# Kernel optimization log

Measured on AMD Instinct MI355X. Metric: run time of the kernel, lower is better.

## Reference

```python
import jax, jax.numpy as jnp
import numpy as np

B = 512
IN_CORES = 12      # input_eff_capsules = 3072/256
N_PRIM = 12        # num_primary_capsules
N_PAR = 10         # num_parent_capsules
RFPC = 4           # receptive fields per capsule = 256/64
RF = 64            # receptive field size
CAP = 256          # capsule size
P_CONN = 0.2


def setup_inputs() -> dict:
    key = jax.random.key(0)
    ks = jax.random.split(key, 16)
    x = jax.random.uniform(ks[0], (B, 32, 32, 3), dtype=jnp.float32)
    # sparse 0/1 routing tensors (fixed Bernoulli(p) connectivity, stored as float params)
    C1 = jax.random.bernoulli(ks[1], P_CONN, (IN_CORES, RFPC, N_PRIM, RFPC)).astype(jnp.float32)
    C_skip = jax.random.bernoulli(ks[2], P_CONN, (IN_CORES, RFPC, N_PAR, RFPC)).astype(jnp.float32)
    C2 = jax.random.bernoulli(ks[3], P_CONN, (N_PRIM, RFPC, N_PAR, RFPC)).astype(jnp.float32)
    # per-receptive-field linear weights of the capsule layers
    s = 1.0 / np.sqrt(RF)
    W1 = jax.random.normal(ks[4], (N_PRIM, RFPC, RF, RF), dtype=jnp.float32) * s
    b1 = jnp.zeros((N_PRIM, RFPC, RF), dtype=jnp.float32)
    W2 = jax.random.normal(ks[5], (N_PAR, RFPC, RF, RF), dtype=jnp.float32) * s
    b2 = jnp.zeros((N_PAR, RFPC, RF), dtype=jnp.float32)
    # reconstruction MLP: 2560 -> 5000 -> 4000 -> 3072
    Wr1 = jax.random.normal(ks[6], (2560, 5000), dtype=jnp.float32) * (1.0 / np.sqrt(2560))
    br1 = jnp.zeros((5000,), dtype=jnp.float32)
    Wr2 = jax.random.normal(ks[7], (5000, 4000), dtype=jnp.float32) * (1.0 / np.sqrt(5000))
    br2 = jnp.zeros((4000,), dtype=jnp.float32)
    Wr3 = jax.random.normal(ks[8], (4000, 3072), dtype=jnp.float32) * (1.0 / np.sqrt(4000))
    br3 = jnp.zeros((3072,), dtype=jnp.float32)
    return {"x": x, "C1": C1, "W1": W1, "b1": b1, "C_skip": C_skip,
            "C2": C2, "W2": W2, "b2": b2,
            "Wr1": Wr1, "br1": br1, "Wr2": Wr2, "br2": br2, "Wr3": Wr3, "br3": br3}


def _caps_layer(x_flat, C, W, b):
    # x_flat: (B, in_cores*RFPC*RF); C: (in_cores, RFPC, out_caps, RFPC)
    bsz = x_flat.shape[0]
    in_cores = C.shape[0]
    xr = x_flat.reshape(bsz, in_cores, RFPC, RF)
    routed = jnp.einsum('ijkl,bijm->bklm', C, xr)          # (B, out_caps, RFPC, RF)
    out = jax.nn.relu(jnp.einsum('bklm,klmn->bkln', routed, W) + b)
    return out.reshape(bsz, -1)


def reference(x, C1, W1, b1, C_skip, C2, W2, b2, Wr1, br1, Wr2, br2, Wr3, br3):
    bsz = x.shape[0]
    # spatial_block_reshape: pure reshapes -> flatten
    x_flat = x.reshape(bsz, -1)                             # (B, 3072)
    # primary capsule layer
    x_prim = _caps_layer(x_flat, C1, W1, b1)                # (B, 3072)
    # skip connection: sparse routing einsum input->parent
    xr = x_prim.reshape(bsz, IN_CORES, RFPC, RF)
    x_skip = jnp.einsum('ijkl,bijm->bklm', C_skip, xr).reshape(bsz, -1)  # (B, 2560)
    # parent capsule layer + skip
    x_sum = x_skip + _caps_layer(x_prim, C2, W2, b2)        # (B, 2560)
    # top-1 capsule mask by norm
    norms = jnp.linalg.norm(x_sum.reshape(bsz, N_PAR, CAP), axis=-1)  # (B, 10)
    active = jnp.argmax(norms, axis=-1)                     # (B,)
    cap_id = jnp.arange(N_PAR * CAP) // CAP                 # (2560,)
    mask = (cap_id[None, :] == active[:, None]).astype(x_sum.dtype)
    x_recon = mask * x_sum
    # reconstruction MLP
    h = jax.nn.relu(x_recon @ Wr1 + br1)
    h = jax.nn.relu(h @ Wr2 + br2)
    out = jax.nn.sigmoid(h @ Wr3 + br3)                     # (B, 3072)
    return (out, x_sum)
```

## Files before the change

### kernel.cpp

```cpp
#include <hip/hip_runtime.h>
#include <math.h>


#define BATCH 512
#define OUT0_SZ (512*3072)

#define LD_XREC 2576
#define LD_H1 5136
#define LD_H2 4112
#define LDP2 4224
#define LDP3 3200
#define SPLITK 4

typedef __attribute__((ext_vector_type(8))) short short8;
typedef __attribute__((ext_vector_type(4))) float f32x4;

__device__ inline unsigned short f2bf(float f) {
    union { float f; unsigned u; } v; v.f = f;
    unsigned r = v.u + 0x7fffu + ((v.u >> 16) & 1u);
    return (unsigned short)(r >> 16);
}
__device__ inline float bf2f(unsigned int hi16) {
    union { unsigned u; float f; } v; v.u = hi16 << 16; return v.f;
}

#define GLD16(g, l) __builtin_amdgcn_global_load_lds( \
    (const __attribute__((address_space(1))) unsigned int*)(g), \
    (__attribute__((address_space(3))) unsigned int*)(l), 16, 0, 0)

struct BReg { float4 r0, r1, r2, r3; };

__device__ inline void loadB(BReg& br, const float* B, int ldB, int Kr, int Nr,
                             int k0, int bn, int tid)
{
    int kq = tid >> 5, f4c = tid & 31;
    int ka = k0 + kq * 4;
    int nb = bn + f4c * 4;
    float4 z = make_float4(0.f, 0.f, 0.f, 0.f);
    br.r0 = z; br.r1 = z; br.r2 = z; br.r3 = z;
    const float* p = B + (size_t)ka * ldB + nb;
    if (nb + 3 < Nr) {
        if (ka + 3 < Kr) {
            br.r0 = *(const float4*)p;
            br.r1 = *(const float4*)(p + ldB);
            br.r2 = *(const float4*)(p + 2 * (size_t)ldB);
            br.r3 = *(const float4*)(p + 3 * (size_t)ldB);
        } else {
            if (ka     < Kr) br.r0 = *(const float4*)p;
            if (ka + 1 < Kr) br.r1 = *(const float4*)(p + ldB);
            if (ka + 2 < Kr) br.r2 = *(const float4*)(p + 2 * (size_t)ldB);
            if (ka + 3 < Kr) br.r3 = *(const float4*)(p + 3 * (size_t)ldB);
        }
    } else {
        float t[4][4] = {};
        #pragma unroll
        for (int e = 0; e < 4; ++e)
            if (ka + e < Kr)
                #pragma unroll
                for (int j = 0; j < 4; ++j)
                    if (nb + j < Nr) t[e][j] = B[(size_t)(ka + e) * ldB + nb + j];
        br.r0 = make_float4(t[0][0], t[0][1], t[0][2], t[0][3]);
        br.r1 = make_float4(t[1][0], t[1][1], t[1][2], t[1][3]);
        br.r2 = make_float4(t[2][0], t[2][1], t[2][2], t[2][3]);
        br.r3 = make_float4(t[3][0], t[3][1], t[3][2], t[3][3]);
    }
}

__device__ inline void writeB(const BReg& br, unsigned short* Bs, int tid)
{
    int kq = tid >> 5, f4c = tid & 31;
    int kqs = kq ^ ((f4c & 3) << 1);
    uint2* B2 = (uint2*)Bs;
    float a0[4] = {br.r0.x, br.r0.y, br.r0.z, br.r0.w};
    float a1[4] = {br.r1.x, br.r1.y, br.r1.z, br.r1.w};
    float a2[4] = {br.r2.x, br.r2.y, br.r2.z, br.r2.w};
    float a3[4] = {br.r3.x, br.r3.y, br.r3.z, br.r3.w};
    #pragma unroll
    for (int j = 0; j < 4; ++j) {
        unsigned int u0 = (unsigned)f2bf(a0[j]) | ((unsigned)f2bf(a1[j]) << 16);
        unsigned int u1 = (unsigned)f2bf(a2[j]) | ((unsigned)f2bf(a3[j]) << 16);
        B2[(f4c * 4 + j) * 10 + kqs] = make_uint2(u0, u1);
    }
}

__device__ inline short8 readB(const unsigned short* Bs, int n, int q)
{
    int sw = ((n >> 2) & 3) << 1;
    return *(const short8*)&Bs[n * 40 + ((2 * q) ^ sw) * 4];
}

__global__ __launch_bounds__(256) void conv_small(
    const float* __restrict__ W1, unsigned short* __restrict__ W1t,
    const float* __restrict__ W2, unsigned short* __restrict__ W2t)
{
    int bid = blockIdx.x;
    const float* W; unsigned short* Wt;
    if (bid < 48) { W = W1 + (size_t)bid * 4096; Wt = W1t + (size_t)bid * 4096; }
    else          { W = W2 + (size_t)(bid - 48) * 4096; Wt = W2t + (size_t)(bid - 48) * 4096; }
    int tid = threadIdx.x;
    int nr = tid >> 2;
    int kc = (tid & 3) * 16;
    float v[16];
    #pragma unroll
    for (int i = 0; i < 16; ++i)
        v[i] = W[(size_t)(kc + i) * 64 + nr];
    unsigned int u[8];
    #pragma unroll
    for (int j = 0; j < 8; ++j)
        u[j] = (unsigned int)f2bf(v[2 * j]) | ((unsigned int)f2bf(v[2 * j + 1]) << 16);
    unsigned int* dst = (unsigned int*)&Wt[(size_t)nr * 64 + kc];
    *(uint4*)(dst)     = make_uint4(u[0], u[1], u[2], u[3]);
    *(uint4*)(dst + 4) = make_uint4(u[4], u[5], u[6], u[7]);
}

__global__ __launch_bounds__(256) void caps_gemm1(
    const float* __restrict__ x, const float* __restrict__ C1,
    const unsigned short* __restrict__ W1t, const float* __restrict__ b1,
    unsigned short* __restrict__ xp)
{
    __shared__ __align__(16) unsigned short As[128 * 72];
    __shared__ __align__(16) unsigned short Bs[64 * 72];
    __shared__ float Csh[48];
    int kl = blockIdx.x;
    int bm = blockIdx.y * 128;
    int tid = threadIdx.x;
    int w = tid >> 6, lane = tid & 63, q = lane >> 4, r16 = lane & 15;
    int wm = (w >> 1) * 64, wn = (w & 1) * 32;

    if (tid < 48) Csh[tid] = C1[tid * 48 + kl];
    {
        const uint4* src = (const uint4*)(W1t + (size_t)kl * 4096);
        #pragma unroll
        for (int p = 0; p < 2; ++p) {
            int c = tid + p * 256;
            int row = c >> 3, cq = c & 7;
            *(uint4*)&Bs[row * 72 + cq * 8] = src[c];
        }
    }
    __syncthreads();

    int arow = tid >> 1, ah = (tid & 1) * 32;
    float accp[32];
    #pragma unroll
    for (int i = 0; i < 32; ++i) accp[i] = 0.f;
    const float* xrow = x + (size_t)(bm + arow) * 3072 + ah;
    for (int ij = 0; ij < 48; ++ij) {
        float c = Csh[ij];
        if (c != 0.f) {
            const float4* p4 = (const float4*)(xrow + ij * 64);
            #pragma unroll
            for (int cc = 0; cc < 8; ++cc) {
                float4 v = p4[cc];
                accp[cc * 4 + 0] = fmaf(c, v.x, accp[cc * 4 + 0]);
                accp[cc * 4 + 1] = fmaf(c, v.y, accp[cc * 4 + 1]);
                accp[cc * 4 + 2] = fmaf(c, v.z, accp[cc * 4 + 2]);
                accp[cc * 4 + 3] = fmaf(c, v.w, accp[cc * 4 + 3]);
            }
        }
    }
    {
        unsigned short* dst = &As[arow * 72 + ah];
        #pragma unroll
        for (int cc = 0; cc < 4; ++cc) {
            unsigned int u[4];
            #pragma unroll
            for (int j = 0; j < 4; ++j)
                u[j] = (unsigned int)f2bf(accp[cc * 8 + 2 * j]) |
                       ((unsigned int)f2bf(accp[cc * 8 + 2 * j + 1]) << 16);
            *(uint4*)&dst[cc * 8] = make_uint4(u[0], u[1], u[2], u[3]);
        }
    }
    __syncthreads();

    f32x4 acc[4][2];
    #pragma unroll
    for (int i = 0; i < 4; ++i)
        #pragma unroll
        for (int j = 0; j < 2; ++j) acc[i][j] = (f32x4)0.f;
    #pragma unroll
    for (int ks = 0; ks < 2; ++ks) {
        short8 a[4], b[2];
        #pragma unroll
        for (int mt = 0; mt < 4; ++mt)
            a[mt] = *(const short8*)&As[(wm + mt * 16 + r16) * 72 + ks * 32 + q * 8];
        #pragma unroll
        for (int nt = 0; nt < 2; ++nt)
            b[nt] = *(const short8*)&Bs[(wn + nt * 16 + r16) * 72 + ks * 32 + q * 8];
        #pragma unroll
        for (int mt = 0; mt < 4; ++mt)
            #pragma unroll
            for (int nt = 0; nt < 2; ++nt)
                acc[mt][nt] = __builtin_amdgcn_mfma_f32_16x16x32_bf16(a[mt], b[nt], acc[mt][nt], 0, 0, 0);
    }

    #pragma unroll
    for (int mt = 0; mt < 4; ++mt) {
        #pragma unroll
        for (int nt = 0; nt < 2; ++nt) {
            int n = wn + nt * 16 + r16;
            float bv = b1[kl * 64 + n];
            #pragma unroll
            for (int reg = 0; reg < 4; ++reg) {
                int row = bm + wm + mt * 16 + q * 4 + reg;
                xp[(size_t)row * 3072 + kl * 64 + n] = f2bf(fmaxf(acc[mt][nt][reg] + bv, 0.f));
            }
        }
    }
}

__global__ __launch_bounds__(256) void caps_gemm2(
    const unsigned short* __restrict__ xp, const float* __restrict__ Cs,
    const float* __restrict__ C2, const unsigned short* __restrict__ W2t,
    const float* __restrict__ b2, float* __restrict__ xsum,
    float* __restrict__ part8)
{
    __shared__ __align__(16) unsigned short As[128 * 72];
    __shared__ __align__(16) unsigned short Bs[64 * 72];
    __shared__ float C2sh[48], Cssh[48];
    int kl = blockIdx.x;
    int bm = blockIdx.y * 128;
    int tid = threadIdx.x;
    int w = tid >> 6, lane = tid & 63, q = lane >> 4, r16 = lane & 15;
    int wm = (w >> 1) * 64, wn = (w & 1) * 32;
    int half = w & 1;

    if (tid < 48) { C2sh[tid] = C2[tid * 40 + kl]; Cssh[tid] = Cs[tid * 40 + kl]; }
    {
        const uint4* src = (const uint4*)(W2t + (size_t)kl * 4096);
        #pragma unroll
        for (int p = 0; p < 2; ++p) {
            int c = tid + p * 256;
            int row = c >> 3, cq = c & 7;
            *(uint4*)&Bs[row * 72 + cq * 8] = src[c];
        }
    }
    __syncthreads();

    int arow = tid >> 1, ah = (tid & 1) * 32;
    float accp[32], skp[32];
    #pragma unroll
    for (int i = 0; i < 32; ++i) { accp[i] = 0.f; skp[i] = 0.f; }
    const unsigned short* xprow = xp + (size_t)(bm + arow) * 3072 + ah;
    for (int ij = 0; ij < 48; ++ij) {
        float c2 = C2sh[ij], cs = Cssh[ij];
        if (c2 != 0.f || cs != 0.f) {
            const uint4* p4 = (const uint4*)(xprow + ij * 64);
            #pragma unroll
            for (int cc = 0; cc < 4; ++cc) {
                uint4 v = p4[cc];
                unsigned int uu[4] = {v.x, v.y, v.z, v.w};
                #pragma unroll
                for (int j = 0; j < 4; ++j) {
                    float lo = bf2f(uu[j] & 0xffffu);
                    float hi = bf2f(uu[j] >> 16);
                    int idx = cc * 8 + 2 * j;
                    accp[idx]     = fmaf(c2, lo, accp[idx]);
                    accp[idx + 1] = fmaf(c2, hi, accp[idx + 1]);
                    skp[idx]      = fmaf(cs, lo, skp[idx]);
                    skp[idx + 1]  = fmaf(cs, hi, skp[idx + 1]);
                }
            }
        }
    }
    {
        unsigned short* dst = &As[arow * 72 + ah];
        #pragma unroll
        for (int cc = 0; cc < 4; ++cc) {
            unsigned int u[4];
            #pragma unroll
            for (int j = 0; j < 4; ++j)
                u[j] = (unsigned int)f2bf(accp[cc * 8 + 2 * j]) |
                       ((unsigned int)f2bf(accp[cc * 8 + 2 * j + 1]) << 16);
            *(uint4*)&dst[cc * 8] = make_uint4(u[0], u[1], u[2], u[3]);
        }
        float* sx = xsum + (size_t)(bm + arow) * 2560 + kl * 64 + ah;
        #pragma unroll
        for (int cc = 0; cc < 8; ++cc)
            *(float4*)&sx[cc * 4] = make_float4(skp[cc*4], skp[cc*4+1], skp[cc*4+2], skp[cc*4+3]);
    }
    __syncthreads();

    f32x4 acc[4][2];
    #pragma unroll
    for (int i = 0; i < 4; ++i)
        #pragma unroll
        for (int j = 0; j < 2; ++j) acc[i][j] = (f32x4)0.f;
    #pragma unroll
    for (int ks = 0; ks < 2; ++ks) {
        short8 a[4], b[2];
        #pragma unroll
        for (int mt = 0; mt < 4; ++mt)
            a[mt] = *(const short8*)&As[(wm + mt * 16 + r16) * 72 + ks * 32 + q * 8];
        #pragma unroll
        for (int nt = 0; nt < 2; ++nt)
            b[nt] = *(const short8*)&Bs[(wn + nt * 16 + r16) * 72 + ks * 32 + q * 8];
        #pragma unroll
        for (int mt = 0; mt < 4; ++mt)
            #pragma unroll
            for (int nt = 0; nt < 2; ++nt)
                acc[mt][nt] = __builtin_amdgcn_mfma_f32_16x16x32_bf16(a[mt], b[nt], acc[mt][nt], 0, 0, 0);
    }

    #pragma unroll
    for (int mt = 0; mt < 4; ++mt) {
        float sreg[4] = {0.f, 0.f, 0.f, 0.f};
        #pragma unroll
        for (int nt = 0; nt < 2; ++nt) {
            int n = wn + nt * 16 + r16;
            float bv = b2[kl * 64 + n];
            #pragma unroll
            for (int reg = 0; reg < 4; ++reg) {
                int lr = wm + mt * 16 + q * 4 + reg;
                size_t xi = (size_t)(bm + lr) * 2560 + kl * 64 + n;
                float v = xsum[xi] + fmaxf(acc[mt][nt][reg] + bv, 0.f);
                xsum[xi] = v;
                sreg[reg] += v * v;
            }
        }
        #pragma unroll
        for (int reg = 0; reg < 4; ++reg) {
            float s = sreg[reg];
            s += __shfl_xor(s, 1); s += __shfl_xor(s, 2);
            s += __shfl_xor(s, 4); s += __shfl_xor(s, 8);
            if (r16 == 0) {
                int row = bm + wm + mt * 16 + q * 4 + reg;
                part8[(size_t)row * 80 + kl * 2 + half] = s;
            }
        }
    }
}

__global__ __launch_bounds__(256) void mask_kernel(
    const float* __restrict__ xs, const float* __restrict__ part8,
    unsigned short* __restrict__ xrec, int* __restrict__ active)
{
    int b = blockIdx.x;
    int tid = threadIdx.x;
    __shared__ float norms[10];
    __shared__ int act_sh;
    if (tid < 10) {
        float s = 0.f;
        #pragma unroll
        for (int j = 0; j < 8; ++j) s += part8[(size_t)b * 80 + tid * 8 + j];
        norms[tid] = s;
    }
    __syncthreads();
    if (tid == 0) {
        int best = 0; float bn = -1.f;
        #pragma unroll
        for (int k = 0; k < 10; ++k)
            if (norms[k] > bn) { bn = norms[k]; best = k; }
        act_sh = best;
        active[b] = best;
    }
    __syncthreads();
    int act = act_sh;
    int idx = act * 256 + tid;
    xrec[(size_t)b * LD_XREC + idx] = f2bf(xs[(size_t)b * 2560 + idx]);
}

__global__ __launch_bounds__(512) void bucket_kernel(
    const int* __restrict__ active, int* __restrict__ perm,
    int4* __restrict__ slots)
{
    __shared__ int cnt[10], pos[10];
    int tid = threadIdx.x;
    if (tid < 10) cnt[tid] = 0;
    __syncthreads();
    int a = active[tid];
    atomicAdd(&cnt[a], 1);
    __syncthreads();
    if (tid == 0) {
        int o = 0, s = 0;
        for (int g = 0; g < 10; ++g) {
            pos[g] = o;
            int mg = cnt[g];
            for (int t0 = 0; t0 < mg; t0 += 64)
                slots[s++] = make_int4(g, o + t0, min(64, mg - t0), 0);
            o += mg;
        }
        for (; s < 18; ++s) slots[s] = make_int4(0, 0, 0, 0);
    }
    __syncthreads();
    int r = atomicAdd(&pos[a], 1);
    perm[r] = tid;
}

__global__ __launch_bounds__(256) void gemm_l1(
    const unsigned short* __restrict__ xrec, const int* __restrict__ perm,
    const int4* __restrict__ slots, const float* __restrict__ Wr1,
    const float* __restrict__ br1, unsigned short* __restrict__ h1)
{
    __shared__ __align__(16) unsigned short As[2][64 * 32];
    __shared__ __align__(16) unsigned short Bs[2][128 * 40];
    __shared__ int rows[64];

    int4 s = slots[blockIdx.y];
    if (s.z == 0) return;
    int g = s.x, mstart = s.y, mval = s.z;
    int bn = blockIdx.x * 128;
    int tid = threadIdx.x;

    if (tid < 64) rows[tid] = perm[mstart + min(tid, mval - 1)];
    __syncthreads();

    int w = tid >> 6, lane = tid & 63;
    int wm = (w >> 1) * 32, wn = (w & 1) * 64;
    int q = lane >> 4, r16 = lane & 15;
    int srow = tid >> 2, skq = tid & 3;

    f32x4 acc[2][4];
    #pragma unroll
    for (int i = 0; i < 2; ++i)
        #pragma unroll
        for (int j = 0; j < 4; ++j) acc[i][j] = (f32x4)0.f;

    int arow = rows[srow];
    const unsigned short* ga = xrec + (size_t)arow * LD_XREC + g * 256 + skq * 8;
    int kbase = g * 256;

    BReg br;
    loadB(br, Wr1, 5000, 2560, 5000, kbase, bn, tid);
    GLD16(ga, &As[0][tid * 8]);
    writeB(br, Bs[0], tid);
    __syncthreads();

    int cur = 0;
    for (int kk = 32; kk <= 256; kk += 32) {
        bool more = kk < 256;
        if (more) {
            GLD16(ga + kk, &As[cur ^ 1][tid * 8]);
            loadB(br, Wr1, 5000, 2560, 5000, kbase + kk, bn, tid);
        }
        short8 a[2], b[4];
        #pragma unroll
        for (int mt = 0; mt < 2; ++mt)
            a[mt] = *(const short8*)&As[cur][(wm + mt * 16 + r16) * 32 + q * 8];
        #pragma unroll
        for (int nt = 0; nt < 4; ++nt)
            b[nt] = readB(Bs[cur], wn + nt * 16 + r16, q);
        #pragma unroll
        for (int mt = 0; mt < 2; ++mt)
            #pragma unroll
            for (int nt = 0; nt < 4; ++nt)
                acc[mt][nt] = __builtin_amdgcn_mfma_f32_16x16x32_bf16(a[mt], b[nt], acc[mt][nt], 0, 0, 0);
        if (more) writeB(br, Bs[cur ^ 1], tid);
        __syncthreads();
        cur ^= 1;
    }

    #pragma unroll
    for (int mt = 0; mt < 2; ++mt) {
        #pragma unroll
        for (int nt = 0; nt < 4; ++nt) {
            int n = bn + wn + nt * 16 + r16;
            float bv = (n < 5000) ? br1[n] : 0.f;
            #pragma unroll
            for (int reg = 0; reg < 4; ++reg) {
                int lm = wm + mt * 16 + q * 4 + reg;
                if (lm < mval)
                    h1[(size_t)(mstart + lm) * LD_H1 + n] =
                        f2bf(fmaxf(acc[mt][nt][reg] + bv, 0.f));
            }
        }
    }
}

__global__ __launch_bounds__(256) void gemm_splitk(
    const unsigned short* __restrict__ A, int ldA,
    const float* __restrict__ B, int ldB, int Kr, int Nr,
    float* __restrict__ P, int ldP, int kper)
{
    __shared__ __align__(16) unsigned short As[2][64 * 32];
    __shared__ __align__(16) unsigned short Bs[2][128 * 40];

    int tid = threadIdx.x;
    int bn = blockIdx.x * 128;
    int bm = blockIdx.y * 64;
    int kz = blockIdx.z * kper;

    int w = tid >> 6, lane = tid & 63;
    int wm = (w >> 1) * 32, wn = (w & 1) * 64;
    int q = lane >> 4, r16 = lane & 15;
    int srow = tid >> 2, skq = tid & 3;

    f32x4 acc[2][4];
    #pragma unroll
    for (int i = 0; i < 2; ++i)
        #pragma unroll
        for (int j = 0; j < 4; ++j) acc[i][j] = (f32x4)0.f;

    const unsigned short* ga = A + (size_t)(bm + srow) * ldA + kz + skq * 8;

    BReg br;
    loadB(br, B, ldB, Kr, Nr, kz, bn, tid);
    GLD16(ga, &As[0][tid * 8]);
    writeB(br, Bs[0], tid);
    __syncthreads();

    int cur = 0;
    for (int kk = 32; kk <= kper; kk += 32) {
        bool more = kk < kper;
        if (more) {
            GLD16(ga + kk, &As[cur ^ 1][tid * 8]);
            loadB(br, B, ldB, Kr, Nr, kz + kk, bn, tid);
        }
        short8 a[2], b[4];
        #pragma unroll
        for (int mt = 0; mt < 2; ++mt)
            a[mt] = *(const short8*)&As[cur][(wm + mt * 16 + r16) * 32 + q * 8];
        #pragma unroll
        for (int nt = 0; nt < 4; ++nt)
            b[nt] = readB(Bs[cur], wn + nt * 16 + r16, q);
        #pragma unroll
        for (int mt = 0; mt < 2; ++mt)
            #pragma unroll
            for (int nt = 0; nt < 4; ++nt)
                acc[mt][nt] = __builtin_amdgcn_mfma_f32_16x16x32_bf16(a[mt], b[nt], acc[mt][nt], 0, 0, 0);
        if (more) writeB(br, Bs[cur ^ 1], tid);
        __syncthreads();
        cur ^= 1;
    }

    float* Pz = P + (size_t)blockIdx.z * 512 * ldP;
    #pragma unroll
    for (int mt = 0; mt < 2; ++mt) {
        #pragma unroll
        for (int nt = 0; nt < 4; ++nt) {
            int cn = bn + wn + nt * 16 + r16;
            #pragma unroll
            for (int reg = 0; reg < 4; ++reg) {
                int cm = bm + wm + mt * 16 + q * 4 + reg;
                Pz[(size_t)cm * ldP + cn] = acc[mt][nt][reg];
            }
        }
    }
}

template<int MODE>
__global__ __launch_bounds__(256) void combine_kernel(
    const float* __restrict__ P, int ldP, const float* __restrict__ bias,
    void* __restrict__ out, int ldO, int Np, int N_real,
    const int* __restrict__ perm)
{
    int gid = blockIdx.x * 256 + threadIdx.x;
    int n0 = (gid * 4) % Np;
    int m  = (gid * 4) / Np;
    size_t MN = (size_t)512 * ldP;
    const float* p = P + (size_t)m * ldP + n0;
    f32x4 s = *(const f32x4*)p;
    s += *(const f32x4*)(p + MN);
    s += *(const f32x4*)(p + 2 * MN);
    s += *(const f32x4*)(p + 3 * MN);
    f32x4 bv = (n0 < N_real) ? *(const f32x4*)(bias + n0) : (f32x4)0.f;
    s += bv;
    if (MODE == 0) {
        unsigned int lo = (unsigned int)f2bf(fmaxf(s[0], 0.f)) | ((unsigned int)f2bf(fmaxf(s[1], 0.f)) << 16);
        unsigned int hi = (unsigned int)f2bf(fmaxf(s[2], 0.f)) | ((unsigned int)f2bf(fmaxf(s[3], 0.f)) << 16);
        *(uint2*)((unsigned short*)out + (size_t)m * ldO + n0) = make_uint2(lo, hi);
    } else {
        int row = perm[m];
        f32x4 v;
        v[0] = 1.f / (1.f + expf(-s[0]));
        v[1] = 1.f / (1.f + expf(-s[1]));
        v[2] = 1.f / (1.f + expf(-s[2]));
        v[3] = 1.f / (1.f + expf(-s[3]));
        *(f32x4*)((float*)out + (size_t)row * ldO + n0) = v;
    }
}

extern "C" void kernel_launch(void* const* d_in, const int* in_sizes, int n_in,
                              void* d_out, int out_size, void* d_ws, size_t ws_size,
                              hipStream_t stream) {
    const float* x   = (const float*)d_in[0];
    const float* C1  = (const float*)d_in[1];
    const float* W1  = (const float*)d_in[2];
    const float* b1  = (const float*)d_in[3];
    const float* Cs  = (const float*)d_in[4];
    const float* C2  = (const float*)d_in[5];
    const float* W2  = (const float*)d_in[6];
    const float* b2  = (const float*)d_in[7];
    const float* Wr1 = (const float*)d_in[8];
    const float* br1 = (const float*)d_in[9];
    const float* Wr2 = (const float*)d_in[10];
    const float* br2 = (const float*)d_in[11];
    const float* Wr3 = (const float*)d_in[12];
    const float* br3 = (const float*)d_in[13];

    float* out = (float*)d_out;
    float* out0     = out;
    float* xsum_out = out + OUT0_SZ;

    char* base = (char*)d_ws;
    unsigned short* xrec = (unsigned short*)(base);
    unsigned short* h1   = (unsigned short*)(base +  2637824);
    unsigned short* h2   = (unsigned short*)(base +  7897088);
    unsigned short* xp   = (unsigned short*)(base + 12107776);
    unsigned short* W1t  = (unsigned short*)(base + 15253504);
    unsigned short* W2t  = (unsigned short*)(base + 15646720);
    float*          part8= (float*)(base + 15974400);
    int*  active = (int*)(base + 16138240);
    int*  perm   = active + 512;
    int4* slots  = (int4*)(perm + 512);
    float*          Pbuf = (float*)(base + 16144384);

    conv_small<<<88, 256, 0, stream>>>(W1, W1t, W2, W2t);

    caps_gemm1<<<dim3(48, 4), 256, 0, stream>>>(x, C1, W1t, b1, xp);
    caps_gemm2<<<dim3(40, 4), 256, 0, stream>>>(xp, Cs, C2, W2t, b2, xsum_out, part8);
    mask_kernel<<<BATCH, 256, 0, stream>>>(xsum_out, part8, xrec, active);
    bucket_kernel<<<1, 512, 0, stream>>>(active, perm, slots);

    gemm_l1<<<dim3(5120 / 128, 18), 256, 0, stream>>>(xrec, perm, slots, Wr1, br1, h1);

    gemm_splitk<<<dim3(4096 / 128, 8, SPLITK), 256, 0, stream>>>(
        h1, LD_H1, Wr2, 4000, 5000, 4000, Pbuf, LDP2, 5120 / SPLITK);
    combine_kernel<0><<<512 * 4096 / 1024, 256, 0, stream>>>(
        Pbuf, LDP2, br2, h2, LD_H2, 4096, 4000, nullptr);

    gemm_splitk<<<dim3(3072 / 128, 8, SPLITK), 256, 0, stream>>>(
        h2, LD_H2, Wr3, 3072, 4000, 3072, Pbuf, LDP3, 4096 / SPLITK);
    combine_kernel<1><<<512 * 3072 / 1024, 256, 0, stream>>>(
        Pbuf, LDP3, br3, out0, 3072, 3072, 3072, perm);
}
```

Measured before the change: 385.7 us.

## Enlarge MLP GEMM tiles to 256x128, split-K 8, XCD-aware mapping, swizzled LDS

Replaces the 64x128 split-K-4 GEMM with a 256x128-tile kernel using split-K 8, a 1D grid mapped so consecutive blocks on the same XCD share N columns, and explicit even/odd B register double-buffering. It also adds XOR swizzles to the A and B shared-memory layouts, including in gemm_l1, to cut LDS bank conflicts. The larger tile raises A/B reuse per load but increases registers (32 accumulators) and doubles the partial-sum traffic the combine kernel must reduce.

```diff
diff --git a/kernel.cpp b/kernel.cpp
--- a/kernel.cpp
+++ b/kernel.cpp
@@ -10,7 +10,7 @@
 #define LD_H2 4112
 #define LDP2 4224
 #define LDP3 3200
-#define SPLITK 4
+#define NZ 8
 
 typedef __attribute__((ext_vector_type(8))) short short8;
 typedef __attribute__((ext_vector_type(4))) float f32x4;
@@ -69,7 +69,7 @@
 __device__ inline void writeB(const BReg& br, unsigned short* Bs, int tid)
 {
     int kq = tid >> 5, f4c = tid & 31;
-    int kqs = kq ^ ((f4c & 3) << 1);
+    int kqs = kq ^ (((f4c >> 1) & 3) << 1);
     uint2* B2 = (uint2*)Bs;
     float a0[4] = {br.r0.x, br.r0.y, br.r0.z, br.r0.w};
     float a1[4] = {br.r1.x, br.r1.y, br.r1.z, br.r1.w};
@@ -85,8 +85,13 @@
 
 __device__ inline short8 readB(const unsigned short* Bs, int n, int q)
 {
-    int sw = ((n >> 2) & 3) << 1;
-    return *(const short8*)&Bs[n * 40 + ((2 * q) ^ sw) * 4];
+    int sw = ((n >> 3) & 3) << 1;
+    return *(const short8*)&Bs[n * 40 + (((2 * q) ^ sw)) * 4];
+}
+
+__device__ inline short8 readA(const unsigned short* As, int row, int q)
+{
+    return *(const short8*)&As[row * 32 + ((q ^ ((row >> 1) & 3)) * 8)];
 }
 
 __global__ __launch_bounds__(256) void conv_small(
@@ -407,7 +412,8 @@
     int w = tid >> 6, lane = tid & 63;
     int wm = (w >> 1) * 32, wn = (w & 1) * 64;
     int q = lane >> 4, r16 = lane & 15;
-    int srow = tid >> 2, skq = tid & 3;
+    int srow = tid >> 2;
+    int akq = (tid & 3) ^ ((srow >> 1) & 3);
 
     f32x4 acc[2][4];
     #pragma unroll
@@ -416,7 +422,7 @@
         for (int j = 0; j < 4; ++j) acc[i][j] = (f32x4)0.f;
 
     int arow = rows[srow];
-    const unsigned short* ga = xrec + (size_t)arow * LD_XREC + g * 256 + skq * 8;
+    const unsigned short* ga = xrec + (size_t)arow * LD_XREC + g * 256 + akq * 8;
     int kbase = g * 256;
 
     BReg br;
@@ -432,18 +438,17 @@
             GLD16(ga + kk, &As[cur ^ 1][tid * 8]);
             loadB(br, Wr1, 5000, 2560, 5000, kbase + kk, bn, tid);
         }
-        short8 a[2], b[4];
-        #pragma unroll
-        for (int mt = 0; mt < 2; ++mt)
-            a[mt] = *(const short8*)&As[cur][(wm + mt * 16 + r16) * 32 + q * 8];
+        short8 b[4];
         #pragma unroll
         for (int nt = 0; nt < 4; ++nt)
             b[nt] = readB(Bs[cur], wn + nt * 16 + r16, q);
         #pragma unroll
-        for (int mt = 0; mt < 2; ++mt)
+        for (int mt = 0; mt < 2; ++mt) {
+            short8 a = readA(As[cur], wm + mt * 16 + r16, q);
             #pragma unroll
             for (int nt = 0; nt < 4; ++nt)
-                acc[mt][nt] = __builtin_amdgcn_mfma_f32_16x16x32_bf16(a[mt], b[nt], acc[mt][nt], 0, 0, 0);
+                acc[mt][nt] = __builtin_amdgcn_mfma_f32_16x16x32_bf16(a, b[nt], acc[mt][nt], 0, 0, 0);
+        }
         if (more) writeB(br, Bs[cur ^ 1], tid);
         __syncthreads();
         cur ^= 1;
@@ -466,65 +471,95 @@
     }
 }
 
-__global__ __launch_bounds__(256) void gemm_splitk(
+__global__ __launch_bounds__(256, 2) void gemm_big(
     const unsigned short* __restrict__ A, int ldA,
     const float* __restrict__ B, int ldB, int Kr, int Nr,
     float* __restrict__ P, int ldP, int kper)
 {
-    __shared__ __align__(16) unsigned short As[2][64 * 32];
+    __shared__ __align__(16) unsigned short As[2][256 * 32];
     __shared__ __align__(16) unsigned short Bs[2][128 * 40];
 
     int tid = threadIdx.x;
-    int bn = blockIdx.x * 128;
-    int bm = blockIdx.y * 64;
-    int kz = blockIdx.z * kper;
+    int bid = blockIdx.x;
+    int xcd = bid & 7;
+    int r   = bid >> 3;
+    int mi  = r & 1;
+    int r2  = r >> 1;
+    int z   = r2 & 7;
+    int bhi = r2 >> 3;
+    int bn = (xcd + 8 * bhi) * 128;
+    int bm = mi * 256;
+    int kz = z * kper;
 
     int w = tid >> 6, lane = tid & 63;
-    int wm = (w >> 1) * 32, wn = (w & 1) * 64;
+    int wm = (w >> 1) * 128, wn = (w & 1) * 64;
     int q = lane >> 4, r16 = lane & 15;
-    int srow = tid >> 2, skq = tid & 3;
-
-    f32x4 acc[2][4];
-    #pragma unroll
-    for (int i = 0; i < 2; ++i)
+
+    f32x4 acc[8][4];
+    #pragma unroll
+    for (int i = 0; i < 8; ++i)
         #pragma unroll
         for (int j = 0; j < 4; ++j) acc[i][j] = (f32x4)0.f;
 
-    const unsigned short* ga = A + (size_t)(bm + srow) * ldA + kz + skq * 8;
-
-    BReg br;
-    loadB(br, B, ldB, Kr, Nr, kz, bn, tid);
-    GLD16(ga, &As[0][tid * 8]);
-    writeB(br, Bs[0], tid);
-    __syncthreads();
-
-    int cur = 0;
-    for (int kk = 32; kk <= kper; kk += 32) {
-        bool more = kk < kper;
-        if (more) {
-            GLD16(ga + kk, &As[cur ^ 1][tid * 8]);
-            loadB(br, B, ldB, Kr, Nr, kz + kk, bn, tid);
-        }
-        short8 a[2], b[4];
-        #pragma unroll
-        for (int mt = 0; mt < 2; ++mt)
-            a[mt] = *(const short8*)&As[cur][(wm + mt * 16 + r16) * 32 + q * 8];
-        #pragma unroll
-        for (int nt = 0; nt < 4; ++nt)
-            b[nt] = readB(Bs[cur], wn + nt * 16 + r16, q);
-        #pragma unroll
-        for (int mt = 0; mt < 2; ++mt)
-            #pragma unroll
-            for (int nt = 0; nt < 4; ++nt)
-                acc[mt][nt] = __builtin_amdgcn_mfma_f32_16x16x32_bf16(a[mt], b[nt], acc[mt][nt], 0, 0, 0);
-        if (more) writeB(br, Bs[cur ^ 1], tid);
+    const unsigned short* ga[4];
+    #pragma unroll
+    for (int p = 0; p < 4; ++p) {
+        int row = (tid >> 2) + p * 64;
+        int kq8 = (tid & 3) ^ ((row >> 1) & 3);
+        ga[p] = A + (size_t)(bm + row) * ldA + kz + kq8 * 8;
+    }
+
+    int nst = kper / 32;
+    BReg brE, brO;
+
+    loadB(brE, B, ldB, Kr, Nr, kz, bn, tid);
+    loadB(brO, B, ldB, Kr, Nr, kz + 32, bn, tid);
+    #pragma unroll
+    for (int p = 0; p < 4; ++p) GLD16(ga[p], &As[0][(tid + p * 256) * 8]);
+    writeB(brE, Bs[0], tid);
+    __syncthreads();
+
+    #define COMPUTE(BUF)                                                      \
+    {                                                                         \
+        short8 b0 = readB(Bs[BUF], wn + r16,      q);                         \
+        short8 b1 = readB(Bs[BUF], wn + 16 + r16, q);                         \
+        short8 b2 = readB(Bs[BUF], wn + 32 + r16, q);                         \
+        short8 b3 = readB(Bs[BUF], wn + 48 + r16, q);                         \
+        _Pragma("unroll")                                                     \
+        for (int mt = 0; mt < 8; ++mt) {                                      \
+            short8 a = readA(As[BUF], wm + mt * 16 + r16, q);                 \
+            acc[mt][0] = __builtin_amdgcn_mfma_f32_16x16x32_bf16(a, b0, acc[mt][0], 0, 0, 0); \
+            acc[mt][1] = __builtin_amdgcn_mfma_f32_16x16x32_bf16(a, b1, acc[mt][1], 0, 0, 0); \
+            acc[mt][2] = __builtin_amdgcn_mfma_f32_16x16x32_bf16(a, b2, acc[mt][2], 0, 0, 0); \
+            acc[mt][3] = __builtin_amdgcn_mfma_f32_16x16x32_bf16(a, b3, acc[mt][3], 0, 0, 0); \
+        }                                                                     \
+    }
+
+    for (int s = 0; s < nst; s += 2) {
+        if (s + 2 < nst) loadB(brE, B, ldB, Kr, Nr, kz + (s + 2) * 32, bn, tid);
+        if (s + 1 < nst) {
+            #pragma unroll
+            for (int p = 0; p < 4; ++p)
+                GLD16(ga[p] + (s + 1) * 32, &As[1][(tid + p * 256) * 8]);
+        }
+        COMPUTE(0);
+        if (s + 1 < nst) writeB(brO, Bs[1], tid);
         __syncthreads();
-        cur ^= 1;
-    }
-
-    float* Pz = P + (size_t)blockIdx.z * 512 * ldP;
-    #pragma unroll
-    for (int mt = 0; mt < 2; ++mt) {
+        if (s + 3 < nst) loadB(brO, B, ldB, Kr, Nr, kz + (s + 3) * 32, bn, tid);
+        if (s + 2 < nst) {
+            #pragma unroll
+            for (int p = 0; p < 4; ++p)
+                GLD16(ga[p] + (s + 2) * 32, &As[0][(tid + p * 256) * 8]);
+        }
+        COMPUTE(1);
+        if (s + 2 < nst) writeB(brE, Bs[0], tid);
+        __syncthreads();
+    }
+    #undef COMPUTE
+
+    float* Pz = P + (size_t)z * 512 * ldP;
+    #pragma unroll
+    for (int mt = 0; mt < 8; ++mt) {
         #pragma unroll
         for (int nt = 0; nt < 4; ++nt) {
             int cn = bn + wn + nt * 16 + r16;
@@ -549,9 +584,9 @@
     size_t MN = (size_t)512 * ldP;
     const float* p = P + (size_t)m * ldP + n0;
     f32x4 s = *(const f32x4*)p;
-    s += *(const f32x4*)(p + MN);
-    s += *(const f32x4*)(p + 2 * MN);
-    s += *(const f32x4*)(p + 3 * MN);
+    #pragma unroll
+    for (int zz = 1; zz < NZ; ++zz)
+        s += *(const f32x4*)(p + (size_t)zz * MN);
     f32x4 bv = (n0 < N_real) ? *(const f32x4*)(bias + n0) : (f32x4)0.f;
     s += bv;
     if (MODE == 0) {
@@ -613,13 +648,11 @@
 
     gemm_l1<<<dim3(5120 / 128, 18), 256, 0, stream>>>(xrec, perm, slots, Wr1, br1, h1);
 
-    gemm_splitk<<<dim3(4096 / 128, 8, SPLITK), 256, 0, stream>>>(
-        h1, LD_H1, Wr2, 4000, 5000, 4000, Pbuf, LDP2, 5120 / SPLITK);
+    gemm_big<<<512, 256, 0, stream>>>(h1, LD_H1, Wr2, 4000, 5000, 4000, Pbuf, LDP2, 640);
     combine_kernel<0><<<512 * 4096 / 1024, 256, 0, stream>>>(
         Pbuf, LDP2, br2, h2, LD_H2, 4096, 4000, nullptr);
 
-    gemm_splitk<<<dim3(3072 / 128, 8, SPLITK), 256, 0, stream>>>(
-        h2, LD_H2, Wr3, 3072, 4000, 3072, Pbuf, LDP3, 4096 / SPLITK);
+    gemm_big<<<384, 256, 0, stream>>>(h2, LD_H2, Wr3, 3072, 4000, 3072, Pbuf, LDP3, 512);
     combine_kernel<1><<<512 * 3072 / 1024, 256, 0, stream>>>(
         Pbuf, LDP3, br3, out0, 3072, 3072, 3072, perm);
 }
```

Measured after the change: 344.7 us. 10.6% less time.
